# Kernel optimization log

Measured on AMD Instinct MI355X. Metric: run time of the kernel, lower is better.

The kernel has to match this reference:

```python
import jax, jax.numpy as jnp
import numpy as np

EPS = 1e-4
GRID_RES = 0.01
L = 2
ATOL = 0.01
RTOL = 1e-5


def compute_lub(f_v, edges):
    # f_v: [V,2] vertex filtration values; edges: [E,2] int vertex indices
    e_x = jnp.max(f_v[:, 0][edges], axis=1)  # [E]
    e_y = jnp.max(f_v[:, 1][edges], axis=1)  # [E]
    f_e = jnp.stack([e_x, e_y], axis=1) + EPS  # [E,2]
    return jnp.concatenate([f_v, f_e], axis=0)  # [V+E, 2] = [S,2]


def grad_matrices(filtration, bar, sample_pts):
    # filtration: [S,2], bar: [P,R], sample_pts: [P,2]
    # Vectorized version of the per-point Python loops in moveSimplices.forward.
    S = filtration.shape[0]
    P = sample_pts.shape[0]
    fx, fy = filtration[:, 0], filtration[:, 1]          # [S]
    px, py = sample_pts[:, 0], sample_pts[:, 1]          # [P]
    fsum = fx + fy                                        # [S]
    psum = px + py                                        # [P]
    shift = jnp.arange(-L, L + 1, dtype=filtration.dtype)  # [5]
    tol_x = ATOL + RTOL * jnp.abs(fx)                     # torch.isclose tolerance
    tol_y = ATOL + RTOL * jnp.abs(fy)
    below = fsum[None, :] < psum[:, None]                 # [P,S]
    above = fsum[None, :] > psum[:, None]

    Gs, Gcs = [], []
    for r in range(bar.shape[1]):  # small fixed rank loop (R=3)
        s = bar[:, r] + GRID_RES                          # [P]
        line_x = shift[None, :] * s[:, None] + px[:, None]  # [P,5]
        line_y = shift[None, :] * s[:, None] + py[:, None]
        last_x, last_y = line_x[:, -1], line_y[:, -1]      # [P] (shift=+L endpoint)
        # isclose over shifts, reduced with any() (duplicate scatter writes are idempotent)
        hit_x = (jnp.abs(line_x[:, None, :] - fx[None, :, None]) <= tol_x[None, :, None]).any(-1)  # [P,S]
        hit_y = (jnp.abs(line_y[:, None, :] - fy[None, :, None]) <= tol_y[None, :, None]).any(-1)
        lx = hit_x & (fy[None, :] <= last_y[:, None]) & below
        ux = hit_x & (fy[None, :] <= last_y[:, None]) & above
        ly = hit_y & (fx[None, :] <= last_x[:, None]) & below
        uy = hit_y & (fx[None, :] <= last_x[:, None]) & above
        vx = ux.astype(filtration.dtype) - lx.astype(filtration.dtype)  # +1 upper, -1 lower (exclusive)
        vy = uy.astype(filtration.dtype) - ly.astype(filtration.dtype)
        G = jnp.stack([vx, vy], axis=-1).reshape(P, 2 * S)  # interleave x,y columns
        cx = jnp.where(ux.any(1), -1.0, jnp.where(lx.any(1), 1.0, 0.0)).astype(filtration.dtype)
        cy = jnp.where(uy.any(1), -1.0, jnp.where(ly.any(1), 1.0, 0.0)).astype(filtration.dtype)
        Gc = jnp.stack([cx, cy], axis=-1)                  # [P,2]
        Gs.append(G)
        Gcs.append(Gc)
    return jnp.stack(Gs), jnp.stack(Gcs)  # [R,P,2S], [R,P,2]


def setup_inputs() -> dict:
    key = jax.random.key(0)
    k1, k2, k3, k4, k5 = jax.random.split(key, 5)
    V, E, P, R = 1200, 4800, 2500, 3
    f_v = jax.random.uniform(k1, (V, 2), dtype=jnp.float32)
    edges = jax.random.randint(k2, (E, 2), 0, V, dtype=jnp.int64)
    bars0 = jax.random.uniform(k3, (P, R), dtype=jnp.float32)
    bars1 = jax.random.uniform(k4, (P, R), dtype=jnp.float32)
    sample_pts = jax.random.uniform(k5, (P, 2), dtype=jnp.float32)
    return {"f_v": f_v, "edges": edges, "bars0": bars0, "bars1": bars1, "sample_pts": sample_pts}


def reference(f_v, edges, bars0, bars1, sample_pts):
    filtration = compute_lub(f_v, edges)
    G0, Gc0 = grad_matrices(filtration, bars0, sample_pts)
    G1, Gc1 = grad_matrices(filtration, bars1, sample_pts)
    # moveSimplices.forward returns the bars unchanged; the grad matrices are the
    # saved side outputs (ctx.grad_matrices_*) and the kernel-heavy computation.
    return (bars0, bars1, G0, G1, Gc0, Gc1)
```

## Files before the change

### kernel.cpp

```cpp
#include <hip/hip_runtime.h>

#define EPS_F      1e-4f
#define GRID_RES_F 0.01f
#define ATOL_F     0.01f
#define RTOL_F     1e-5f

static constexpr int V = 1200;
static constexpr int E = 4800;
static constexpr int S = V + E;
static constexpr int P = 2500;
static constexpr int R = 3;
static constexpr int PB = 4;

static constexpr size_t G0_BASE  = 15000ull;
static constexpr size_t ROW_LEN  = 2ull * S;
static constexpr size_t G_ELEMS  = (size_t)R * P * ROW_LEN;
static constexpr size_t GC0_BASE = G0_BASE + 2 * G_ELEMS;

__global__ void build_filt_kernel(const float* __restrict__ f_v,
                                  const int*   __restrict__ edges,
                                  float4*      __restrict__ filt) {
    int j = blockIdx.x * blockDim.x + threadIdx.x;
    if (j >= S) return;
    float fx, fy;
    if (j < V) {
        fx = f_v[2 * j];
        fy = f_v[2 * j + 1];
    } else {
        int e = j - V;
        int a = edges[2 * e];
        int b = edges[2 * e + 1];
        fx = __fadd_rn(fmaxf(f_v[2 * a],     f_v[2 * b]),     EPS_F);
        fy = __fadd_rn(fmaxf(f_v[2 * a + 1], f_v[2 * b + 1]), EPS_F);
    }
    float tolx = __fadd_rn(ATOL_F, __fmul_rn(RTOL_F, fabsf(fx)));
    float toly = __fadd_rn(ATOL_F, __fmul_rn(RTOL_F, fabsf(fy)));
    filt[j] = make_float4(fx, fy, tolx, toly);
}

__device__ __forceinline__ float mindist(const float* l, float f) {
    float a = fabsf(__fsub_rn(l[0], f));
    float b = fabsf(__fsub_rn(l[1], f));
    float c = fabsf(__fsub_rn(l[2], f));
    float d = fabsf(__fsub_rn(l[3], f));
    float e = fabsf(__fsub_rn(l[4], f));
    return fminf(fminf(fminf(a, b), fminf(c, d)), e);
}

__device__ __forceinline__ void cell(const float4& f, float psum,
                                     const float* lxs, const float* lys,
                                     float& vx, float& vy,
                                     int& aux, int& alx, int& auy, int& aly) {
    float fsum = __fadd_rn(f.x, f.y);
    bool ab = fsum > psum, be = fsum < psum;
    float sg = ab ? 1.0f : (be ? -1.0f : 0.0f);
    bool cx = (mindist(lxs, f.x) <= f.z) && (f.y <= lys[4]);
    bool cy = (mindist(lys, f.y) <= f.w) && (f.x <= lxs[4]);
    vx = cx ? sg : 0.0f;
    vy = cy ? sg : 0.0f;
    aux |= (int)(cx && ab); alx |= (int)(cx && be);
    auy |= (int)(cy && ab); aly |= (int)(cy && be);
}

__global__ __launch_bounds__(256) void grad_kernel(
        const float4* __restrict__ filt,
        const float*  __restrict__ bars0,
        const float*  __restrict__ bars1,
        const float*  __restrict__ sample_pts,
        float*        __restrict__ d_out) {
    const int r = blockIdx.y;
    const int b = blockIdx.z;
    const float* bar = (b == 0) ? bars0 : bars1;
    const int p0 = blockIdx.x * PB;

    __shared__ int shw[4][4];

    for (int pp = 0; pp < PB; ++pp) {
        const int p = p0 + pp;

        const float px = sample_pts[2 * p];
        const float py = sample_pts[2 * p + 1];
        const float psum = __fadd_rn(px, py);
        const float s  = __fadd_rn(bar[p * R + r], GRID_RES_F);
        const float s2 = __fmul_rn(2.0f, s);

        float lxs[5], lys[5];
        lxs[0] = __fadd_rn(-s2, px); lxs[1] = __fadd_rn(-s, px); lxs[2] = px;
        lxs[3] = __fadd_rn( s, px);  lxs[4] = __fadd_rn(s2, px);
        lys[0] = __fadd_rn(-s2, py); lys[1] = __fadd_rn(-s, py); lys[2] = py;
        lys[3] = __fadd_rn( s, py);  lys[4] = __fadd_rn(s2, py);

        float* Grow = d_out + G0_BASE + (size_t)b * G_ELEMS
                            + ((size_t)(r * P + p)) * ROW_LEN;

        int aux = 0, alx = 0, auy = 0, aly = 0;

        int j = threadIdx.x * 4;
        float4 a0, a1, a2, a3;
        if (j < S) { a0 = filt[j]; a1 = filt[j+1]; a2 = filt[j+2]; a3 = filt[j+3]; }
        while (j < S) {
            const int jn = j + 1024;
            float4 b0, b1, b2, b3;
            if (jn < S) {
                b0 = filt[jn]; b1 = filt[jn+1]; b2 = filt[jn+2]; b3 = filt[jn+3];
            }
            float4 o0, o1;
            cell(a0, psum, lxs, lys, o0.x, o0.y, aux, alx, auy, aly);
            cell(a1, psum, lxs, lys, o0.z, o0.w, aux, alx, auy, aly);
            cell(a2, psum, lxs, lys, o1.x, o1.y, aux, alx, auy, aly);
            cell(a3, psum, lxs, lys, o1.z, o1.w, aux, alx, auy, aly);
            float4* dst = reinterpret_cast<float4*>(Grow + 2 * j);
            dst[0] = o0;
            dst[1] = o1;
            a0 = b0; a1 = b1; a2 = b2; a3 = b3;
            j = jn;
        }

        const int lane = threadIdx.x & 63;
        const int wid  = threadIdx.x >> 6;
        int f0 = __any(aux), f1 = __any(alx), f2 = __any(auy), f3 = __any(aly);
        if (lane == 0) {
            shw[wid][0] = f0; shw[wid][1] = f1; shw[wid][2] = f2; shw[wid][3] = f3;
        }
        __syncthreads();
        if (threadIdx.x == 0) {
            int ux = shw[0][0] | shw[1][0] | shw[2][0] | shw[3][0];
            int lx = shw[0][1] | shw[1][1] | shw[2][1] | shw[3][1];
            int uy = shw[0][2] | shw[1][2] | shw[2][2] | shw[3][2];
            int ly = shw[0][3] | shw[1][3] | shw[2][3] | shw[3][3];
            float cx = ux ? -1.0f : (lx ? 1.0f : 0.0f);
            float cy = uy ? -1.0f : (ly ? 1.0f : 0.0f);
            size_t gc = GC0_BASE + (size_t)b * ((size_t)R * P * 2)
                                 + ((size_t)(r * P + p)) * 2;
            d_out[gc]     = cx;
            d_out[gc + 1] = cy;
        }
        __syncthreads();
    }
}

extern "C" void kernel_launch(void* const* d_in, const int* in_sizes, int n_in,
                              void* d_out, int out_size, void* d_ws, size_t ws_size,
                              hipStream_t stream) {
    const float* f_v        = (const float*)d_in[0];
    const int*   edges      = (const int*)d_in[1];
    const float* bars0      = (const float*)d_in[2];
    const float* bars1      = (const float*)d_in[3];
    const float* sample_pts = (const float*)d_in[4];
    float* out = (float*)d_out;

    float4* filt = (float4*)d_ws;

    (void)hipMemcpyAsync(out,         bars0, (size_t)P * R * sizeof(float),
                         hipMemcpyDeviceToDevice, stream);
    (void)hipMemcpyAsync(out + P * R, bars1, (size_t)P * R * sizeof(float),
                         hipMemcpyDeviceToDevice, stream);

    build_filt_kernel<<<(S + 255) / 256, 256, 0, stream>>>(f_v, edges, filt);

    grad_kernel<<<dim3(P / PB, R, 2), 256, 0, stream>>>(filt, bars0, bars1,
                                                        sample_pts, out);
}
```

Baseline: 733.1 us.

## Use one row per block with nontemporal coalesced float4 stores

Each block now handles a single sample point row instead of four, removing the per-row loop and barriers and quadrupling the grid size. Each lane processes two adjacent cells at two offsets so that wave stores are contiguous 16-byte chunks, and the output is written with nontemporal stores to avoid polluting cache with the write-only matrix. This costs repeated per-block setup and re-reads of the filtration table for every row.

```diff
diff --git a/kernel.cpp b/kernel.cpp
--- a/kernel.cpp
+++ b/kernel.cpp
@@ -10,7 +10,8 @@
 static constexpr int S = V + E;
 static constexpr int P = 2500;
 static constexpr int R = 3;
-static constexpr int PB = 4;
+
+typedef float v4f __attribute__((ext_vector_type(4)));
 
 static constexpr size_t G0_BASE  = 15000ull;
 static constexpr size_t ROW_LEN  = 2ull * S;
@@ -68,74 +69,79 @@
         const float*  __restrict__ bars1,
         const float*  __restrict__ sample_pts,
         float*        __restrict__ d_out) {
+    const int p = blockIdx.x;
     const int r = blockIdx.y;
     const int b = blockIdx.z;
+
     const float* bar = (b == 0) ? bars0 : bars1;
-    const int p0 = blockIdx.x * PB;
+    const float px = sample_pts[2 * p];
+    const float py = sample_pts[2 * p + 1];
+    const float psum = __fadd_rn(px, py);
+    const float s  = __fadd_rn(bar[p * R + r], GRID_RES_F);
+    const float s2 = __fmul_rn(2.0f, s);
+
+    float lxs[5], lys[5];
+    lxs[0] = __fadd_rn(-s2, px); lxs[1] = __fadd_rn(-s, px); lxs[2] = px;
+    lxs[3] = __fadd_rn( s, px);  lxs[4] = __fadd_rn(s2, px);
+    lys[0] = __fadd_rn(-s2, py); lys[1] = __fadd_rn(-s, py); lys[2] = py;
+    lys[3] = __fadd_rn( s, py);  lys[4] = __fadd_rn(s2, py);
+
+    float* Grow = d_out + G0_BASE + (size_t)b * G_ELEMS
+                        + ((size_t)(r * P + p)) * ROW_LEN;
 
     __shared__ int shw[4][4];
+    const int lane = threadIdx.x & 63;
+    const int wv   = threadIdx.x >> 6;
 
-    for (int pp = 0; pp < PB; ++pp) {
-        const int p = p0 + pp;
+    int aux = 0, alx = 0, auy = 0, aly = 0;
 
-        const float px = sample_pts[2 * p];
-        const float py = sample_pts[2 * p + 1];
-        const float psum = __fadd_rn(px, py);
-        const float s  = __fadd_rn(bar[p * R + r], GRID_RES_F);
-        const float s2 = __fmul_rn(2.0f, s);
+    int c0 = wv * 256 + 2 * lane;
+    int c1 = c0 + 128;
+    float4 a0 = {}, a1 = {}, a2 = {}, a3 = {};
+    if (c0 < S) { a0 = filt[c0]; a1 = filt[c0 + 1]; }
+    if (c1 < S) { a2 = filt[c1]; a3 = filt[c1 + 1]; }
+    while (c0 < S) {
+        const int c0n = c0 + 1024, c1n = c1 + 1024;
+        float4 b0 = {}, b1 = {}, b2 = {}, b3 = {};
+        if (c0n < S) { b0 = filt[c0n]; b1 = filt[c0n + 1]; }
+        if (c1n < S) { b2 = filt[c1n]; b3 = filt[c1n + 1]; }
 
-        float lxs[5], lys[5];
-        lxs[0] = __fadd_rn(-s2, px); lxs[1] = __fadd_rn(-s, px); lxs[2] = px;
-        lxs[3] = __fadd_rn( s, px);  lxs[4] = __fadd_rn(s2, px);
-        lys[0] = __fadd_rn(-s2, py); lys[1] = __fadd_rn(-s, py); lys[2] = py;
-        lys[3] = __fadd_rn( s, py);  lys[4] = __fadd_rn(s2, py);
+        {
+            float ox, oy, oz, ow;
+            cell(a0, psum, lxs, lys, ox, oy, aux, alx, auy, aly);
+            cell(a1, psum, lxs, lys, oz, ow, aux, alx, auy, aly);
+            v4f o; o.x = ox; o.y = oy; o.z = oz; o.w = ow;
+            __builtin_nontemporal_store(o,
+                reinterpret_cast<v4f*>(Grow + 2 * (size_t)c0));
+        }
+        if (c1 < S) {
+            float ox, oy, oz, ow;
+            cell(a2, psum, lxs, lys, ox, oy, aux, alx, auy, aly);
+            cell(a3, psum, lxs, lys, oz, ow, aux, alx, auy, aly);
+            v4f o; o.x = ox; o.y = oy; o.z = oz; o.w = ow;
+            __builtin_nontemporal_store(o,
+                reinterpret_cast<v4f*>(Grow + 2 * (size_t)c1));
+        }
+        a0 = b0; a1 = b1; a2 = b2; a3 = b3;
+        c0 = c0n; c1 = c1n;
+    }
 
-        float* Grow = d_out + G0_BASE + (size_t)b * G_ELEMS
-                            + ((size_t)(r * P + p)) * ROW_LEN;
-
-        int aux = 0, alx = 0, auy = 0, aly = 0;
-
-        int j = threadIdx.x * 4;
-        float4 a0, a1, a2, a3;
-        if (j < S) { a0 = filt[j]; a1 = filt[j+1]; a2 = filt[j+2]; a3 = filt[j+3]; }
-        while (j < S) {
-            const int jn = j + 1024;
-            float4 b0, b1, b2, b3;
-            if (jn < S) {
-                b0 = filt[jn]; b1 = filt[jn+1]; b2 = filt[jn+2]; b3 = filt[jn+3];
-            }
-            float4 o0, o1;
-            cell(a0, psum, lxs, lys, o0.x, o0.y, aux, alx, auy, aly);
-            cell(a1, psum, lxs, lys, o0.z, o0.w, aux, alx, auy, aly);
-            cell(a2, psum, lxs, lys, o1.x, o1.y, aux, alx, auy, aly);
-            cell(a3, psum, lxs, lys, o1.z, o1.w, aux, alx, auy, aly);
-            float4* dst = reinterpret_cast<float4*>(Grow + 2 * j);
-            dst[0] = o0;
-            dst[1] = o1;
-            a0 = b0; a1 = b1; a2 = b2; a3 = b3;
-            j = jn;
-        }
-
-        const int lane = threadIdx.x & 63;
-        const int wid  = threadIdx.x >> 6;
-        int f0 = __any(aux), f1 = __any(alx), f2 = __any(auy), f3 = __any(aly);
-        if (lane == 0) {
-            shw[wid][0] = f0; shw[wid][1] = f1; shw[wid][2] = f2; shw[wid][3] = f3;
-        }
-        __syncthreads();
-        if (threadIdx.x == 0) {
-            int ux = shw[0][0] | shw[1][0] | shw[2][0] | shw[3][0];
-            int lx = shw[0][1] | shw[1][1] | shw[2][1] | shw[3][1];
-            int uy = shw[0][2] | shw[1][2] | shw[2][2] | shw[3][2];
-            int ly = shw[0][3] | shw[1][3] | shw[2][3] | shw[3][3];
-            float cx = ux ? -1.0f : (lx ? 1.0f : 0.0f);
-            float cy = uy ? -1.0f : (ly ? 1.0f : 0.0f);
-            size_t gc = GC0_BASE + (size_t)b * ((size_t)R * P * 2)
-                                 + ((size_t)(r * P + p)) * 2;
-            d_out[gc]     = cx;
-            d_out[gc + 1] = cy;
-        }
-        __syncthreads();
+    int f0 = __any(aux), f1 = __any(alx), f2 = __any(auy), f3 = __any(aly);
+    if (lane == 0) {
+        shw[wv][0] = f0; shw[wv][1] = f1; shw[wv][2] = f2; shw[wv][3] = f3;
+    }
+    __syncthreads();
+    if (threadIdx.x == 0) {
+        int ux = shw[0][0] | shw[1][0] | shw[2][0] | shw[3][0];
+        int lx = shw[0][1] | shw[1][1] | shw[2][1] | shw[3][1];
+        int uy = shw[0][2] | shw[1][2] | shw[2][2] | shw[3][2];
+        int ly = shw[0][3] | shw[1][3] | shw[2][3] | shw[3][3];
+        float cx = ux ? -1.0f : (lx ? 1.0f : 0.0f);
+        float cy = uy ? -1.0f : (ly ? 1.0f : 0.0f);
+        size_t gc = GC0_BASE + (size_t)b * ((size_t)R * P * 2)
+                             + ((size_t)(r * P + p)) * 2;
+        d_out[gc]     = cx;
+        d_out[gc + 1] = cy;
     }
 }
 
@@ -158,6 +164,6 @@
 
     build_filt_kernel<<<(S + 255) / 256, 256, 0, stream>>>(f_v, edges, filt);
 
-    grad_kernel<<<dim3(P / PB, R, 2), 256, 0, stream>>>(filt, bars0, bars1,
-                                                        sample_pts, out);
+    grad_kernel<<<dim3(P, R, 2), 256, 0, stream>>>(filt, bars0, bars1,
+                                                   sample_pts, out);
 }
```

Result: slower. 772.7 us (+5.4%).
